# Kernel tuning notes

Hardware: AMD Instinct MI355X
Metric: run time of the kernel (lower is better)

The kernel has to match this reference:

```python
import jax, jax.numpy as jnp
import numpy as np

_N = 2048          # matrix_size (A_sparse.shape[0] in the original)
_NNZ = 32768       # number of factor / pred entries
_LOGCOND_EPS = 1e-12


def setup_inputs() -> dict:
    key = jax.random.key(0)
    k1, k2, k3, k4, k5 = jax.random.split(key, 5)
    pred_values = jax.random.normal(k1, (_NNZ,), dtype=jnp.float32)
    active_scales = jax.random.uniform(k2, (_NNZ,), dtype=jnp.float32) * 0.05
    A_factor = jax.random.normal(k3, (_N, _N), dtype=jnp.float32)
    factor_rows = jax.random.randint(k4, (_NNZ,), 0, _N, dtype=jnp.int32)
    factor_cols = jax.random.randint(k5, (_NNZ,), 0, _N, dtype=jnp.int32)
    return {
        "pred_values": pred_values,
        "active_scales": active_scales,
        "A_factor": A_factor,
        "factor_rows": factor_rows,
        "factor_cols": factor_cols,
    }


def reference(pred_values, active_scales, A_factor, factor_rows, factor_cols):
    n = A_factor.shape[0]
    dt = pred_values.dtype
    # SPD system matrix A (stands in for the original fixed A_sparse)
    A = A_factor @ A_factor.T / jnp.asarray(n, dt) + jnp.eye(n, dtype=dt)
    # Sparse factor L assembled from predicted values (scatter-add, dup-safe),
    # unit diagonal keeps L A L^T well conditioned / SPD.
    L = jnp.eye(n, dtype=dt).at[factor_rows, factor_cols].add(pred_values * active_scales)
    # Preconditioned matrix M = L A L^T (symmetric PSD)
    M = L @ A @ L.T
    M = 0.5 * (M + M.T)
    evals = jnp.linalg.eigvalsh(M)  # ascending
    lam_min = jnp.maximum(evals[0], _LOGCOND_EPS)
    lam_max = jnp.maximum(evals[-1], _LOGCOND_EPS)
    # loss = log(lambda_max) - log(lambda_min) = log condition number
    return jnp.log(lam_max) - jnp.log(lam_min)
```

## Files before the change

### kernel.cpp

```cpp
#include <hip/hip_runtime.h>

#define N2 2048
#define NNZ 32768
#define LK 22
#define NBL 128
#define BINCAP 64

typedef __attribute__((ext_vector_type(8))) _Float16 half8;
typedef __attribute__((ext_vector_type(4))) float f32x4;

#define AGENT __HIP_MEMORY_SCOPE_AGENT
#define AS1C(p) ((const __attribute__((address_space(1))) unsigned int*)(p))
#define AS3(p)  ((__attribute__((address_space(3))) unsigned int*)(p))

__device__ __forceinline__ unsigned short f2h(float f) {
  _Float16 h = (_Float16)f;
  return *(unsigned short*)&h;
}
__device__ __forceinline__ float h2f(unsigned short u) {
  _Float16 h = *(_Float16*)&u;
  return (float)h;
}


__global__ __launch_bounds__(256) void convert_kernel(const float* __restrict__ W,
                                                      unsigned short* __restrict__ Hf,
                                                      unsigned* __restrict__ cntR,
                                                      unsigned* __restrict__ cntC) {
  if (blockIdx.x < 8)       cntR[blockIdx.x * 256 + threadIdx.x] = 0;
  else if (blockIdx.x < 16) cntC[(blockIdx.x - 8) * 256 + threadIdx.x] = 0;
  int i4 = blockIdx.x * 256 + threadIdx.x;
  float4 w = ((const float4*)W)[i4];
  ushort4 h;
  h.x = f2h(w.x); h.y = f2h(w.y); h.z = f2h(w.z); h.w = f2h(w.w);
  ((ushort4*)Hf)[i4] = h;
}

__global__ __launch_bounds__(256) void fill_kernel(const float* __restrict__ pred,
                                                   const float* __restrict__ scal,
                                                   const int* __restrict__ rows,
                                                   const int* __restrict__ cols,
                                                   unsigned* __restrict__ cntR,
                                                   int* __restrict__ binRc,
                                                   float* __restrict__ binRv,
                                                   unsigned* __restrict__ cntC,
                                                   int* __restrict__ binCr,
                                                   float* __restrict__ binCv) {
  int k = blockIdx.x * 256 + threadIdx.x;
  int r = rows[k], c = cols[k];
  float v = pred[k] * scal[k];
  unsigned pR = atomicAdd(&cntR[r], 1u);
  if (pR < BINCAP) { binRc[r * BINCAP + pR] = c; binRv[r * BINCAP + pR] = v; }
  unsigned pC = atomicAdd(&cntC[c], 1u);
  if (pC < BINCAP) { binCr[c * BINCAP + pC] = r; binCv[c * BINCAP + pC] = v; }
}

__global__ __launch_bounds__(256) void gatherG_kernel(const unsigned* __restrict__ cntR,
                                                      const int* __restrict__ binRc,
                                                      const float* __restrict__ binRv,
                                                      const unsigned short* __restrict__ Hf,
                                                      unsigned short* __restrict__ Gh) {
  const int r = blockIdx.x, tid = threadIdx.x;
  __shared__ int scol_[BINCAP];
  __shared__ float sval_[BINCAP];
  const unsigned ne = min(cntR[r], (unsigned)BINCAP);
  if (tid < ne) {
    scol_[tid] = binRc[r * BINCAP + tid];
    sval_[tid] = binRv[r * BINCAP + tid];
  }
  __syncthreads();
  uint4 own = *(const uint4*)(Hf + (size_t)r * 2048 + tid * 8);
  half8 ho = *(half8*)&own;
  float acc[8];
#pragma unroll
  for (int k = 0; k < 8; ++k) acc[k] = (float)ho[k];
  unsigned e = 0;
  for (; e + 8 <= ne; e += 8) {
    uint4 q[8];
#pragma unroll
    for (int u = 0; u < 8; ++u)
      q[u] = *(const uint4*)(Hf + (size_t)scol_[e + u] * 2048 + tid * 8);
#pragma unroll
    for (int u = 0; u < 8; ++u) {
      half8 hv = *(half8*)&q[u];
      const float v = sval_[e + u];
#pragma unroll
      for (int k = 0; k < 8; ++k) acc[k] += v * (float)hv[k];
    }
  }
  for (; e + 4 <= ne; e += 4) {
    uint4 q[4];
#pragma unroll
    for (int u = 0; u < 4; ++u)
      q[u] = *(const uint4*)(Hf + (size_t)scol_[e + u] * 2048 + tid * 8);
#pragma unroll
    for (int u = 0; u < 4; ++u) {
      half8 hv = *(half8*)&q[u];
      const float v = sval_[e + u];
#pragma unroll
      for (int k = 0; k < 8; ++k) acc[k] += v * (float)hv[k];
    }
  }
  for (; e < ne; ++e) {
    uint4 qq = *(const uint4*)(Hf + (size_t)scol_[e] * 2048 + tid * 8);
    half8 hv = *(half8*)&qq;
    const float v = sval_[e];
#pragma unroll
    for (int k = 0; k < 8; ++k) acc[k] += v * (float)hv[k];
  }
  unsigned short o[8];
#pragma unroll
  for (int k = 0; k < 8; ++k) o[k] = f2h(acc[k]);
  *(uint4*)(Gh + (size_t)r * 2048 + tid * 8) = *(uint4*)o;
}

__device__ __forceinline__ void stage_tiles2(const unsigned short* __restrict__ X,
                                             unsigned short* Xb, unsigned short* Yb,
                                             int row0, int col0, int kk,
                                             int srowX, int srowY, int scol, int wq) {
  __builtin_amdgcn_global_load_lds(
      AS1C(X + (size_t)(row0 + srowX) * 2048 + kk + scol),
      AS3(Xb + (wq * 16) * 32), 16, 0, 0);
#pragma unroll
  for (int q = 0; q < 2; ++q) {
    __builtin_amdgcn_global_load_lds(
        AS1C(X + (size_t)(col0 + srowY + q * 16) * 2048 + kk + scol),
        AS3(Yb + (wq * 32 + q * 16) * 32), 16, 0, 0);
  }
}

__global__ __launch_bounds__(512) void gemmM_kernel(const unsigned short* __restrict__ Gh,
                                                    float* __restrict__ M) {
  const int tid = threadIdx.x;
  int bi, bj;
  bool diag;
  if (blockIdx.x < 32) {
    bi = blockIdx.x; bj = bi >> 1; diag = true;
  } else {
    int idx = blockIdx.x - 32;
    int j = 0;
    while (j < 14 && idx >= (j + 1) * (30 - j)) ++j;
    bj = j;
    bi = 2 * j + 2 + (idx - j * (31 - j));
    diag = false;
  }

  __shared__ __align__(16) char smem[49152];
  unsigned short* Xs = (unsigned short*)smem;
  unsigned short* Ys = (unsigned short*)(smem + 16384);
  float* Cred = (float*)smem;

  const int w = tid >> 6, lane = tid & 63;
  const int half = w >> 2, wq = w & 3;
  const int row0 = bi * 64, col0 = bj * 128;
  const int m0 = (wq & 1) * 32, n0 = (wq >> 1) * 64;
  f32x4 acc[2][4];
#pragma unroll
  for (int a = 0; a < 2; ++a)
#pragma unroll
    for (int b = 0; b < 4; ++b) acc[a][b] = (f32x4){0.f, 0.f, 0.f, 0.f};
  const int mrow = lane & 15, kseg = (lane >> 4) * 8;
  const int srowX = wq * 16 + (lane >> 2);
  const int srowY = wq * 32 + (lane >> 2);
  const int scol = (lane & 3) * 8;
  const int kbase = half * 1024;

  stage_tiles2(Gh, Xs + (half * 2 + 0) * 2048, Ys + (half * 2 + 0) * 4096,
               row0, col0, kbase, srowX, srowY, scol, wq);
  for (int t = 0; t < 32; ++t) {
    const int cur = t & 1;
    __syncthreads();
    if (t < 31)
      stage_tiles2(Gh, Xs + (half * 2 + (cur ^ 1)) * 2048,
                   Ys + (half * 2 + (cur ^ 1)) * 4096,
                   row0, col0, kbase + (t + 1) * 32, srowX, srowY, scol, wq);
    const unsigned short* Xb = Xs + (half * 2 + cur) * 2048;
    const unsigned short* Yb = Ys + (half * 2 + cur) * 4096;
    half8 af[2], bf[4];
#pragma unroll
    for (int q = 0; q < 2; ++q)
      af[q] = *(const half8*)(Xb + (m0 + q * 16 + mrow) * 32 + kseg);
#pragma unroll
    for (int q = 0; q < 4; ++q)
      bf[q] = *(const half8*)(Yb + (n0 + q * 16 + mrow) * 32 + kseg);
#pragma unroll
    for (int mt = 0; mt < 2; ++mt)
#pragma unroll
      for (int nt = 0; nt < 4; ++nt)
        acc[mt][nt] = __builtin_amdgcn_mfma_f32_16x16x32_f16(af[mt], bf[nt], acc[mt][nt], 0, 0, 0);
  }
  const int crow = (lane >> 4) * 4, ccol = lane & 15;
  __syncthreads();
  if (half == 1) {
#pragma unroll
    for (int mt = 0; mt < 2; ++mt)
#pragma unroll
      for (int nt = 0; nt < 4; ++nt)
#pragma unroll
        for (int r = 0; r < 4; ++r)
          Cred[(m0 + mt * 16 + crow + r) * 132 + n0 + nt * 16 + ccol] = acc[mt][nt][r];
  }
  __syncthreads();
  if (half == 0) {
    const float invn = 1.0f / 2048.0f;
#pragma unroll
    for (int mt = 0; mt < 2; ++mt)
#pragma unroll
      for (int nt = 0; nt < 4; ++nt) {
        const int gi0 = row0 + m0 + mt * 16 + crow;
        const int gj = col0 + n0 + nt * 16 + ccol;
        size_t base = (size_t)gi0 * 2048 + gj;
#pragma unroll
        for (int r = 0; r < 4; ++r) {
          const int li = (m0 + mt * 16 + crow + r) * 132 + n0 + nt * 16 + ccol;
          float val = (acc[mt][nt][r] + Cred[li]) * invn +
                      ((gi0 + r == gj) ? 1.0f : 0.0f);
          M[base + (size_t)r * 2048] = val;
          if (!diag) Cred[li] = val;
        }
      }
  }
  if (!diag) {
    __syncthreads();
    const int orow = tid >> 2;
    const int cseg = (tid & 3) * 16;
    float mv[16];
#pragma unroll
    for (int k = 0; k < 16; ++k)
      mv[k] = Cred[(cseg + k) * 132 + orow];
    float4* dst = (float4*)(M + (size_t)(col0 + orow) * 2048 + row0 + cseg);
    dst[0] = (float4){mv[0], mv[1], mv[2], mv[3]};
    dst[1] = (float4){mv[4], mv[5], mv[6], mv[7]};
    dst[2] = (float4){mv[8], mv[9], mv[10], mv[11]};
    dst[3] = (float4){mv[12], mv[13], mv[14], mv[15]};
  }
}

__global__ __launch_bounds__(256) void scatterS_kernel(const float* __restrict__ pred,
                                                       const float* __restrict__ scal,
                                                       const int* __restrict__ rows,
                                                       const int* __restrict__ cols,
                                                       const unsigned* __restrict__ cntC,
                                                       const int* __restrict__ binCr,
                                                       const float* __restrict__ binCv,
                                                       float* __restrict__ M) {
  const int tid = threadIdx.x;
  if (blockIdx.x < 128) {
    int k = blockIdx.x * 256 + tid;
    int r = rows[k], c = cols[k];
    float v = pred[k] * scal[k];
    atomicAdd(&M[(size_t)r * 2048 + c], v);
    atomicAdd(&M[(size_t)c * 2048 + r], v);
    return;
  }
  const int c = blockIdx.x - 128;
  __shared__ int rr_[BINCAP];
  __shared__ float vv_[BINCAP];
  const unsigned nc = min(cntC[c], (unsigned)BINCAP);
  if (tid < nc) {
    rr_[tid] = binCr[c * BINCAP + tid];
    vv_[tid] = binCv[c * BINCAP + tid];
  }
  __syncthreads();
  const unsigned np = nc * nc;
  for (unsigned p = tid; p < np; p += 256) {
    unsigned i1 = p / nc, i2 = p - i1 * nc;
    atomicAdd(&M[(size_t)rr_[i1] * 2048 + rr_[i2]], vv_[i1] * vv_[i2]);
  }
}

__device__ __forceinline__ float block_sum8(float v, float* red) {
#pragma unroll
  for (int off = 32; off; off >>= 1) v += __shfl_down(v, off);
  if ((threadIdx.x & 63) == 0) red[threadIdx.x >> 6] = v;
  __syncthreads();
  float r = ((red[0] + red[1]) + (red[2] + red[3])) +
            ((red[4] + red[5]) + (red[6] + red[7]));
  __syncthreads();
  return r;
}

__global__ __launch_bounds__(512) void lanczos_kernel(const float* __restrict__ M,
                                                      unsigned long long* __restrict__ Z0,
                                                      unsigned long long* __restrict__ Z1,
                                                      float* __restrict__ out) {
  const int tid = threadIdx.x, b = blockIdx.x;
  const int wave = tid >> 6, lane = tid & 63;
  __shared__ __align__(16) float Mlds[16 * 2048];
  __shared__ __align__(16) float VA[2048];
  __shared__ __align__(16) float VB[2048];
  __shared__ float red[8];
  __shared__ float al[LK + 2], b2[LK + 2];
  __shared__ float bnds[2], res[2];

  const float* Mblk = M + (size_t)b * 16 * 2048;
#pragma unroll
  for (int q = 0; q < 16; ++q)
    __builtin_amdgcn_global_load_lds(AS1C(Mblk + wave * 4096 + q * 256 + lane * 4),
                                     AS3(Mlds + wave * 4096 + q * 256), 16, 0, 0);

  float pv[4];
  float part = 0.f;
#pragma unroll
  for (int t = 0; t < 4; ++t) {
    int i = t * 512 + tid;
    unsigned u = (unsigned)i * 2654435761u;
    u ^= u >> 16; u *= 2246822519u; u ^= u >> 13;
    float rv = (float)(u >> 8) * (2.f / 16777216.f) - 1.f;
    pv[t] = rv;
    part += rv * rv;
  }
  float nrm = block_sum8(part, red);
  float innm = rsqrtf(nrm);
#pragma unroll
  for (int t = 0; t < 4; ++t) {
    int i = t * 512 + tid;
    VA[i] = pv[t] * innm;
    VB[i] = 0.f;
  }
  __syncthreads();

  float* Vcur = VA;
  float* Vprev = VB;
  float beta_prev = 0.f;

  for (int j = 1; j <= LK; ++j) {
    unsigned long long* Z = (j & 1) ? Z0 : Z1;
#pragma unroll
    for (int rr = 0; rr < 2; ++rr) {
      const int r = b * 16 + wave * 2 + rr;
      const float4* Mr = (const float4*)(Mlds + (wave * 2 + rr) * 2048);
      float s = 0.f;
#pragma unroll
      for (int t = 0; t < 8; ++t) {
        int idx = t * 64 + lane;
        float4 m4 = Mr[idx];
        float4 v4 = ((const float4*)Vcur)[idx];
        s += m4.x * v4.x + m4.y * v4.y + m4.z * v4.z + m4.w * v4.w;
      }
#pragma unroll
      for (int off = 32; off; off >>= 1) s += __shfl_down(s, off);
      if (lane == 0) {
        float zv = s - beta_prev * Vprev[r];
        unsigned long long pk = ((unsigned long long)(unsigned)j << 32) |
                                (unsigned long long)(unsigned)__float_as_uint(zv);
        __hip_atomic_store(&Z[r], pk, __ATOMIC_RELAXED, AGENT);
      }
    }

    float va[4];
#pragma unroll
    for (int t = 0; t < 4; ++t) va[t] = Vcur[t * 512 + tid];

    unsigned long long w4[4];
    int rounds = 0;
    for (;;) {
      bool ok = true;
#pragma unroll
      for (int t = 0; t < 4; ++t) {
        w4[t] = __hip_atomic_load(&Z[t * 512 + tid], __ATOMIC_RELAXED, AGENT);
        ok &= ((unsigned)(w4[t] >> 32) == (unsigned)j);
      }
      if (ok) break;
      if (rounds == 1)      __builtin_amdgcn_s_sleep(1);
      else if (rounds == 2) __builtin_amdgcn_s_sleep(2);
      else if (rounds >= 3) __builtin_amdgcn_s_sleep(8);
      ++rounds;
    }
    float za[4];
    float pa = 0.f;
#pragma unroll
    for (int t = 0; t < 4; ++t) {
      za[t] = __uint_as_float((unsigned)w4[t]);
      pa += za[t] * va[t];
    }
    float alpha = block_sum8(pa, red);
    float pb = 0.f;
#pragma unroll
    for (int t = 0; t < 4; ++t) {
      float rsd = za[t] - alpha * va[t];
      pb += rsd * rsd;
    }
    float beta2 = block_sum8(pb, red);
    float beta = sqrtf(fmaxf(beta2, 1e-30f));
    float invb = 1.f / beta;
    if (tid == 0) { al[j] = alpha; b2[j] = beta2; }
#pragma unroll
    for (int t = 0; t < 4; ++t) {
      int i = t * 512 + tid;
      Vprev[i] = (za[t] - alpha * va[t]) * invb;
    }
    float* tmp = Vprev; Vprev = Vcur; Vcur = tmp;
    beta_prev = beta;
    __syncthreads();
  }

  if (b == 0) {
    if (tid == 0) {
      float lo = 1e30f, hi = -1e30f;
      for (int i = 1; i <= LK; ++i) {
        float bl = (i > 1) ? sqrtf(b2[i - 1]) : 0.f;
        float br = (i < LK) ? sqrtf(b2[i]) : 0.f;
        lo = fminf(lo, al[i] - bl - br);
        hi = fmaxf(hi, al[i] + bl + br);
      }
      bnds[0] = lo; bnds[1] = hi;
    }
    __syncthreads();
    if (wave < 2) {
      const int tcount = (wave == 0) ? 1 : LK;
      float lo = bnds[0], hi = bnds[1];
      for (int round = 0; round < 4; ++round) {
        float x = lo + (hi - lo) * (float)(lane + 1) * (1.f / 65.f);
        int cnt = 0;
        float d = al[1] - x;
        if (fabsf(d) < 1e-25f) d = -1e-25f;
        if (d < 0.f) cnt++;
        for (int i = 2; i <= LK; ++i) {
          d = (al[i] - x) - b2[i - 1] / d;
          if (fabsf(d) < 1e-25f) d = -1e-25f;
          if (d < 0.f) cnt++;
        }
        bool ab = (cnt >= tcount);
        float cand_hi = ab ? x : hi;
        float cand_lo = ab ? lo : x;
#pragma unroll
        for (int off = 32; off; off >>= 1) {
          cand_hi = fminf(cand_hi, __shfl_down(cand_hi, off));
          cand_lo = fmaxf(cand_lo, __shfl_down(cand_lo, off));
        }
        cand_hi = __shfl(cand_hi, 0);
        cand_lo = __shfl(cand_lo, 0);
        hi = cand_hi;
        lo = fminf(cand_lo, hi);
      }
      if (lane == 0) res[wave] = 0.5f * (lo + hi);
    }
    __syncthreads();
    if (tid == 0) {
      float lmin = fmaxf(res[0], 1e-12f);
      float lmax = fmaxf(res[1], 1e-12f);
      out[0] = logf(lmax) - logf(lmin);
    }
  }
}

extern "C" void kernel_launch(void* const* d_in, const int* in_sizes, int n_in,
                              void* d_out, int out_size, void* d_ws, size_t ws_size,
                              hipStream_t stream) {
  const float* pred = (const float*)d_in[0];
  const float* scal = (const float*)d_in[1];
  const float* W    = (const float*)d_in[2];
  const int*   rows = (const int*)d_in[3];
  const int*   cols = (const int*)d_in[4];
  float* out = (float*)d_out;

  char* ws = (char*)d_ws;
  const size_t MB = 1024 * 1024;
  unsigned short* Hf = (unsigned short*)(ws);
  unsigned short* Gh = (unsigned short*)(ws + 8 * MB);
  float* M = (float*)(ws + 16 * MB);
  char* ctrl = ws + 32 * MB;
  unsigned* cntR = (unsigned*)(ctrl);
  unsigned* cntC = (unsigned*)(ctrl + 8192);
  int*      binRc = (int*)(ctrl + 16384);
  float*    binRv = (float*)(ctrl + 16384 + 524288);
  int*      binCr = (int*)(ctrl + 16384 + 2 * 524288);
  float*    binCv = (float*)(ctrl + 16384 + 3 * 524288);
  unsigned long long* Z0 = (unsigned long long*)(ctrl + 16384 + 4 * 524288);
  unsigned long long* Z1 = (unsigned long long*)(ctrl + 16384 + 4 * 524288 + 16384);

  convert_kernel<<<4096, 256, 0, stream>>>(W, Hf, cntR, cntC);
  fill_kernel<<<NNZ / 256, 256, 0, stream>>>(pred, scal, rows, cols,
                                             cntR, binRc, binRv, cntC, binCr, binCv);
  gatherG_kernel<<<2048, 256, 0, stream>>>(cntR, binRc, binRv, Hf, Gh);
  gemmM_kernel<<<272, 512, 0, stream>>>(Gh, M);
  scatterS_kernel<<<2176, 256, 0, stream>>>(pred, scal, rows, cols,
                                            cntC, binCr, binCv, M);

  lanczos_kernel<<<NBL, 512, 0, stream>>>(M, Z0, Z1, out);
}
```

Baseline: 267.3 us.

## Fuse sparse-term scatter into Lanczos kernel via LDS atomics on resident rows

Removes the separate scatterS kernel, which used global atomics to add the sparse L terms and the S·S^T outer products into M. Each Lanczos block now adds those contributions straight into its LDS-resident rows, using the row and column bins. This saves one launch and a global atomic pass over M. In exchange the Lanczos prologue gets longer and serial: each row loops over its entries and gathers column bins, which adds latency before the iteration starts.

```diff
diff --git a/kernel.cpp b/kernel.cpp
--- a/kernel.cpp
+++ b/kernel.cpp
@@ -16,10 +16,6 @@
 __device__ __forceinline__ unsigned short f2h(float f) {
   _Float16 h = (_Float16)f;
   return *(unsigned short*)&h;
-}
-__device__ __forceinline__ float h2f(unsigned short u) {
-  _Float16 h = *(_Float16*)&u;
-  return (float)h;
 }
 
 
@@ -236,39 +232,6 @@
   }
 }
 
-__global__ __launch_bounds__(256) void scatterS_kernel(const float* __restrict__ pred,
-                                                       const float* __restrict__ scal,
-                                                       const int* __restrict__ rows,
-                                                       const int* __restrict__ cols,
-                                                       const unsigned* __restrict__ cntC,
-                                                       const int* __restrict__ binCr,
-                                                       const float* __restrict__ binCv,
-                                                       float* __restrict__ M) {
-  const int tid = threadIdx.x;
-  if (blockIdx.x < 128) {
-    int k = blockIdx.x * 256 + tid;
-    int r = rows[k], c = cols[k];
-    float v = pred[k] * scal[k];
-    atomicAdd(&M[(size_t)r * 2048 + c], v);
-    atomicAdd(&M[(size_t)c * 2048 + r], v);
-    return;
-  }
-  const int c = blockIdx.x - 128;
-  __shared__ int rr_[BINCAP];
-  __shared__ float vv_[BINCAP];
-  const unsigned nc = min(cntC[c], (unsigned)BINCAP);
-  if (tid < nc) {
-    rr_[tid] = binCr[c * BINCAP + tid];
-    vv_[tid] = binCv[c * BINCAP + tid];
-  }
-  __syncthreads();
-  const unsigned np = nc * nc;
-  for (unsigned p = tid; p < np; p += 256) {
-    unsigned i1 = p / nc, i2 = p - i1 * nc;
-    atomicAdd(&M[(size_t)rr_[i1] * 2048 + rr_[i2]], vv_[i1] * vv_[i2]);
-  }
-}
-
 __device__ __forceinline__ float block_sum8(float v, float* red) {
 #pragma unroll
   for (int off = 32; off; off >>= 1) v += __shfl_down(v, off);
@@ -281,6 +244,12 @@
 }
 
 __global__ __launch_bounds__(512) void lanczos_kernel(const float* __restrict__ M,
+                                                      const unsigned* __restrict__ cntR,
+                                                      const int* __restrict__ binRc,
+                                                      const float* __restrict__ binRv,
+                                                      const unsigned* __restrict__ cntC,
+                                                      const int* __restrict__ binCr,
+                                                      const float* __restrict__ binCv,
                                                       unsigned long long* __restrict__ Z0,
                                                       unsigned long long* __restrict__ Z1,
                                                       float* __restrict__ out) {
@@ -317,6 +286,25 @@
     int i = t * 512 + tid;
     VA[i] = pv[t] * innm;
     VB[i] = 0.f;
+  }
+  __syncthreads();
+
+  for (int rr = 0; rr < 2; ++rr) {
+    const int r = b * 16 + wave * 2 + rr;
+    float* Mrow = Mlds + (wave * 2 + rr) * 2048;
+    const unsigned nR = min(cntR[r], (unsigned)BINCAP);
+    for (unsigned e = lane; e < nR; e += 64)
+      atomicAdd(&Mrow[binRc[r * BINCAP + e]], binRv[r * BINCAP + e]);
+    const unsigned nC = min(cntC[r], (unsigned)BINCAP);
+    for (unsigned e = lane; e < nC; e += 64)
+      atomicAdd(&Mrow[binCr[r * BINCAP + e]], binCv[r * BINCAP + e]);
+    for (unsigned e = 0; e < nR; ++e) {
+      const int c = binRc[r * BINCAP + e];
+      const float v = binRv[r * BINCAP + e];
+      const unsigned nc2 = min(cntC[c], (unsigned)BINCAP);
+      for (unsigned p = lane; p < nc2; p += 64)
+        atomicAdd(&Mrow[binCr[c * BINCAP + p]], v * binCv[c * BINCAP + p]);
+    }
   }
   __syncthreads();
 
@@ -475,8 +463,6 @@
                                              cntR, binRc, binRv, cntC, binCr, binCv);
   gatherG_kernel<<<2048, 256, 0, stream>>>(cntR, binRc, binRv, Hf, Gh);
   gemmM_kernel<<<272, 512, 0, stream>>>(Gh, M);
-  scatterS_kernel<<<2176, 256, 0, stream>>>(pred, scal, rows, cols,
-                                            cntC, binCr, binCv, M);
-
-  lanczos_kernel<<<NBL, 512, 0, stream>>>(M, Z0, Z1, out);
-}
+  lanczos_kernel<<<NBL, 512, 0, stream>>>(M, cntR, binRc, binRv,
+                                          cntC, binCr, binCv, Z0, Z1, out);
+}
```

After: 267.4 us. Within noise of the previous version (+0.1%).
